# Optimization experiments

Measured on AMD Instinct MI355X. Metric: run time of the kernel, lower is better.

The kernel has to match this reference:

```python
import jax, jax.numpy as jnp
import numpy as np

NOISE_STD = 0.5
NOISE_VAR = NOISE_STD ** 2  # softmax temperature = 1 / noise_variance

N, C, H, W = 256, 3, 32, 32
M = 50000


def setup_inputs() -> dict:
    key = jax.random.key(0)
    k1, k2 = jax.random.split(key)
    x = jax.random.normal(k1, (N, C, H, W), dtype=jnp.float32)
    dataset = jax.random.normal(k2, (M, C, H, W), dtype=jnp.float32)
    return {"x": x, "dataset": dataset}


def reference(x, dataset):
    # Flatten: x -> [N, D], dataset -> [M, D]
    n = x.shape[0]
    input_shape = dataset.shape[1:]
    xf = x.reshape(n, -1)
    df = dataset.reshape(dataset.shape[0], -1)
    # scores = x . dataset^T / noise_variance, softmax over dataset axis
    scores = jnp.einsum("nd,md->nm", xf, df) / NOISE_VAR  # [N, M]
    w = jax.nn.softmax(scores, axis=-1)
    # Weighted average of dataset points: [N, D]
    out = jnp.einsum("nm,md->nd", w, df)
    return out.reshape((n,) + input_shape)
```

## Files before the change

### kernel.cpp

```cpp
#include <hip/hip_runtime.h>
#include <stdint.h>
#include <stddef.h>

#define N_Q 256
#define M_D 50000
#define K_D 3072
#define MTILE 64
#define BK 32
#define CAND_CAP 128
#define WINDOW 9.0f

typedef short bf16x8 __attribute__((ext_vector_type(8)));
typedef float f32x4 __attribute__((ext_vector_type(4)));

static __device__ inline unsigned short f2bf(float f) {
    unsigned int u = __float_as_uint(f);
    u += 0x7fffu + ((u >> 16) & 1u);
    return (unsigned short)(u >> 16);
}

__global__ __launch_bounds__(256) void cvt_x_kernel(const float* __restrict__ x,
                                                    short* __restrict__ xb) {
    int i = (blockIdx.x * 256 + threadIdx.x) * 4;
    float4 f = *(const float4*)(x + i);
    ushort4 o;
    o.x = f2bf(f.x); o.y = f2bf(f.y); o.z = f2bf(f.z); o.w = f2bf(f.w);
    *(ushort4*)(xb + i) = o;
}

__global__ __launch_bounds__(256) void gemm_scores(const short* __restrict__ xb,
                                                   const float* __restrict__ dset,
                                                   float* __restrict__ scores) {
    __shared__ __align__(16) short sA[N_Q * BK];
    __shared__ __align__(16) short sB[MTILE * BK];

    const int tid = threadIdx.x;
    const int w = tid >> 6;
    const int l = tid & 63;
    const int m0 = blockIdx.x * MTILE;

    f32x4 acc[4][4];
#pragma unroll
    for (int i = 0; i < 4; ++i)
#pragma unroll
        for (int j = 0; j < 4; ++j)
            acc[i][j] = (f32x4){0.f, 0.f, 0.f, 0.f};

    const int br = tid >> 2;
    const int bq = tid & 3;
    const bool bvalid = (m0 + br) < M_D;
    const float* bsrc = dset + (size_t)(m0 + br) * K_D + bq * 8;

    const int kk = (l >> 4) * 8;
    const int rA = l & 15;

    for (int kt = 0; kt < K_D / BK; ++kt) {
        __syncthreads();

#pragma unroll
        for (int j = 0; j < 4; ++j) {
            int c = j * 256 + tid;
            int row = c >> 2;
            int off = c & 3;
            bf16x8 v = *(const bf16x8*)(xb + (size_t)row * K_D + kt * BK + off * 8);
            *(bf16x8*)&sA[c * 8] = v;
        }
        {
            bf16x8 pk;
            if (bvalid) {
                const float* p = bsrc + kt * BK;
                float4 f0 = *(const float4*)p;
                float4 f1 = *(const float4*)(p + 4);
                pk[0] = (short)f2bf(f0.x); pk[1] = (short)f2bf(f0.y);
                pk[2] = (short)f2bf(f0.z); pk[3] = (short)f2bf(f0.w);
                pk[4] = (short)f2bf(f1.x); pk[5] = (short)f2bf(f1.y);
                pk[6] = (short)f2bf(f1.z); pk[7] = (short)f2bf(f1.w);
            } else {
                pk = (bf16x8){0, 0, 0, 0, 0, 0, 0, 0};
            }
            *(bf16x8*)&sB[br * BK + bq * 8] = pk;
        }
        __syncthreads();

        bf16x8 af[4], bfr[4];
#pragma unroll
        for (int ai = 0; ai < 4; ++ai)
            af[ai] = *(const bf16x8*)&sA[(w * 64 + ai * 16 + rA) * BK + kk];
#pragma unroll
        for (int bj = 0; bj < 4; ++bj)
            bfr[bj] = *(const bf16x8*)&sB[(bj * 16 + rA) * BK + kk];
#pragma unroll
        for (int ai = 0; ai < 4; ++ai)
#pragma unroll
            for (int bj = 0; bj < 4; ++bj)
                acc[ai][bj] = __builtin_amdgcn_mfma_f32_16x16x32_bf16(
                    af[ai], bfr[bj], acc[ai][bj], 0, 0, 0);
    }

    const int crow = (l >> 4) * 4;
    const int ccol = l & 15;
#pragma unroll
    for (int ai = 0; ai < 4; ++ai) {
#pragma unroll
        for (int bj = 0; bj < 4; ++bj) {
            int m = m0 + bj * 16 + ccol;
            if (m < M_D) {
#pragma unroll
                for (int r = 0; r < 4; ++r) {
                    int n = w * 64 + ai * 16 + crow + r;
                    scores[(size_t)n * M_D + m] = acc[ai][bj][r];
                }
            }
        }
    }
}

__global__ __launch_bounds__(256) void scan_rows(const float* __restrict__ scores,
                                                 int* __restrict__ cidx,
                                                 int* __restrict__ ccnt) {
    const int n = blockIdx.x;
    const int tid = threadIdx.x;
    const float4* row4 = (const float4*)(scores + (size_t)n * M_D);

    float mx = -3.0e38f;
    for (int m4 = tid; m4 < M_D / 4; m4 += 256) {
        float4 v = row4[m4];
        mx = fmaxf(mx, fmaxf(fmaxf(v.x, v.y), fmaxf(v.z, v.w)));
    }
#pragma unroll
    for (int off = 32; off > 0; off >>= 1) mx = fmaxf(mx, __shfl_down(mx, off));

    __shared__ float wred[4];
    __shared__ int cnt;
    if ((tid & 63) == 0) wred[tid >> 6] = mx;
    if (tid == 0) cnt = 0;
    __syncthreads();
    float rowmax = fmaxf(fmaxf(wred[0], wred[1]), fmaxf(wred[2], wred[3]));
    float thr = rowmax - WINDOW;

    for (int m4 = tid; m4 < M_D / 4; m4 += 256) {
        float4 v = row4[m4];
        if (v.x >= thr || v.y >= thr || v.z >= thr || v.w >= thr) {
            float e[4] = {v.x, v.y, v.z, v.w};
#pragma unroll
            for (int j = 0; j < 4; ++j) {
                if (e[j] >= thr) {
                    int p = atomicAdd(&cnt, 1);
                    if (p < CAND_CAP) cidx[n * CAND_CAP + p] = m4 * 4 + j;
                }
            }
        }
    }
    __syncthreads();
    if (tid == 0) ccnt[n] = cnt < CAND_CAP ? cnt : CAND_CAP;
}

__global__ __launch_bounds__(256) void finalize_rows(const float* __restrict__ x,
                                                     const float* __restrict__ dset,
                                                     const int* __restrict__ cidx,
                                                     const int* __restrict__ ccnt,
                                                     float* __restrict__ out) {
    const int n = blockIdx.x;
    const int tid = threadIdx.x;
    const int cnt = ccnt[n];

    __shared__ float L[CAND_CAP];
    __shared__ float wred[4];
    const float4* xr4 = (const float4*)(x + (size_t)n * K_D);

    for (int c = 0; c < cnt; ++c) {
        const float4* dr4 = (const float4*)(dset + (size_t)cidx[n * CAND_CAP + c] * K_D);
        float p = 0.f;
        for (int j = tid; j < K_D / 4; j += 256) {
            float4 a = xr4[j], b = dr4[j];
            p += a.x * b.x + a.y * b.y + a.z * b.z + a.w * b.w;
        }
#pragma unroll
        for (int off = 32; off > 0; off >>= 1) p += __shfl_down(p, off);
        if ((tid & 63) == 0) wred[tid >> 6] = p;
        __syncthreads();
        if (tid == 0) L[c] = 4.0f * (wred[0] + wred[1] + wred[2] + wred[3]);
        __syncthreads();
    }

    if (tid == 0) {
        float mx = -3.0e38f;
        for (int c = 0; c < cnt; ++c) mx = fmaxf(mx, L[c]);
        float s = 0.f;
        for (int c = 0; c < cnt; ++c) { float e = expf(L[c] - mx); L[c] = e; s += e; }
        float inv = 1.0f / s;
        for (int c = 0; c < cnt; ++c) L[c] *= inv;
    }
    __syncthreads();

    float4* out4 = (float4*)(out + (size_t)n * K_D);
    for (int j = tid; j < K_D / 4; j += 256) {
        float4 o = {0.f, 0.f, 0.f, 0.f};
        for (int c = 0; c < cnt; ++c) {
            float wc = L[c];
            float4 d = *(const float4*)(dset + (size_t)cidx[n * CAND_CAP + c] * K_D + j * 4);
            o.x += wc * d.x; o.y += wc * d.y; o.z += wc * d.z; o.w += wc * d.w;
        }
        out4[j] = o;
    }
}

extern "C" void kernel_launch(void* const* d_in, const int* in_sizes, int n_in,
                              void* d_out, int out_size, void* d_ws, size_t ws_size,
                              hipStream_t stream) {
    const float* x = (const float*)d_in[0];
    const float* dset = (const float*)d_in[1];
    float* out = (float*)d_out;

    char* ws = (char*)d_ws;
    short* xb = (short*)ws;
    float* scores = (float*)(ws + 1572864);
    int* cidx = (int*)(ws + 1572864 + 51200000);
    int* ccnt = (int*)(ws + 1572864 + 51200000 + 131072);

    cvt_x_kernel<<<768, 256, 0, stream>>>(x, xb);
    gemm_scores<<<(M_D + MTILE - 1) / MTILE, 256, 0, stream>>>(xb, dset, scores);
    scan_rows<<<N_Q, 256, 0, stream>>>(scores, cidx, ccnt);
    finalize_rows<<<N_Q, 256, 0, stream>>>(x, dset, cidx, ccnt, out);
}
```

Before: 961.5 us.

## Load A tile via global_load_lds, prefetch B before sync, fuse scan and finalize

The GEMM now loads the bf16 query tile straight from global memory into LDS with global_load_lds instead of staging it through registers. The dataset float loads are issued at the start of each k-iteration, and the barrier sits after the MFMAs so load latency overlaps the previous wait. The scan and finalize kernels are merged into one, with candidate indices kept in shared memory instead of a workspace buffer. This removes a kernel launch and the global round-trip for the candidate lists. The LDS layout for A has to match the lane-to-row mapping of global_load_lds, and correctness depends on it.

```diff
diff --git a/kernel.cpp b/kernel.cpp
--- a/kernel.cpp
+++ b/kernel.cpp
@@ -13,6 +13,9 @@
 typedef short bf16x8 __attribute__((ext_vector_type(8)));
 typedef float f32x4 __attribute__((ext_vector_type(4)));
 
+typedef const __attribute__((address_space(1))) void* gptr_as1;
+typedef __attribute__((address_space(3))) void* lptr_as3;
+
 static __device__ inline unsigned short f2bf(float f) {
     unsigned int u = __float_as_uint(f);
     u += 0x7fffu + ((u >> 16) & 1u);
@@ -51,26 +54,29 @@
     const bool bvalid = (m0 + br) < M_D;
     const float* bsrc = dset + (size_t)(m0 + br) * K_D + bq * 8;
 
+    const int arow_base = w * 16 + (l >> 2);
+    const int acol = (l & 3) * 8;
+
     const int kk = (l >> 4) * 8;
     const int rA = l & 15;
 
     for (int kt = 0; kt < K_D / BK; ++kt) {
-        __syncthreads();
-
+        float4 f0, f1;
+        if (bvalid) {
+            const float* p = bsrc + kt * BK;
+            f0 = *(const float4*)p;
+            f1 = *(const float4*)(p + 4);
+        }
 #pragma unroll
         for (int j = 0; j < 4; ++j) {
-            int c = j * 256 + tid;
-            int row = c >> 2;
-            int off = c & 3;
-            bf16x8 v = *(const bf16x8*)(xb + (size_t)row * K_D + kt * BK + off * 8);
-            *(bf16x8*)&sA[c * 8] = v;
+            const short* gp = xb + (size_t)(j * 64 + arow_base) * K_D + kt * BK + acol;
+            __builtin_amdgcn_global_load_lds((gptr_as1)gp,
+                                             (lptr_as3)(sA + j * 2048 + w * 512),
+                                             16, 0, 0);
         }
         {
             bf16x8 pk;
             if (bvalid) {
-                const float* p = bsrc + kt * BK;
-                float4 f0 = *(const float4*)p;
-                float4 f1 = *(const float4*)(p + 4);
                 pk[0] = (short)f2bf(f0.x); pk[1] = (short)f2bf(f0.y);
                 pk[2] = (short)f2bf(f0.z); pk[3] = (short)f2bf(f0.w);
                 pk[4] = (short)f2bf(f1.x); pk[5] = (short)f2bf(f1.y);
@@ -95,6 +101,7 @@
             for (int bj = 0; bj < 4; ++bj)
                 acc[ai][bj] = __builtin_amdgcn_mfma_f32_16x16x32_bf16(
                     af[ai], bfr[bj], acc[ai][bj], 0, 0, 0);
+        __syncthreads();
     }
 
     const int crow = (l >> 4) * 4;
@@ -115,12 +122,18 @@
     }
 }
 
-__global__ __launch_bounds__(256) void scan_rows(const float* __restrict__ scores,
-                                                 int* __restrict__ cidx,
-                                                 int* __restrict__ ccnt) {
+__global__ __launch_bounds__(256) void scan_finalize(const float* __restrict__ scores,
+                                                     const float* __restrict__ x,
+                                                     const float* __restrict__ dset,
+                                                     float* __restrict__ out) {
     const int n = blockIdx.x;
     const int tid = threadIdx.x;
     const float4* row4 = (const float4*)(scores + (size_t)n * M_D);
+
+    __shared__ float wred[4];
+    __shared__ int cnt;
+    __shared__ int cid[CAND_CAP];
+    __shared__ float L[CAND_CAP];
 
     float mx = -3.0e38f;
     for (int m4 = tid; m4 < M_D / 4; m4 += 256) {
@@ -129,9 +142,6 @@
     }
 #pragma unroll
     for (int off = 32; off > 0; off >>= 1) mx = fmaxf(mx, __shfl_down(mx, off));
-
-    __shared__ float wred[4];
-    __shared__ int cnt;
     if ((tid & 63) == 0) wred[tid >> 6] = mx;
     if (tid == 0) cnt = 0;
     __syncthreads();
@@ -146,30 +156,17 @@
             for (int j = 0; j < 4; ++j) {
                 if (e[j] >= thr) {
                     int p = atomicAdd(&cnt, 1);
-                    if (p < CAND_CAP) cidx[n * CAND_CAP + p] = m4 * 4 + j;
+                    if (p < CAND_CAP) cid[p] = m4 * 4 + j;
                 }
             }
         }
     }
     __syncthreads();
-    if (tid == 0) ccnt[n] = cnt < CAND_CAP ? cnt : CAND_CAP;
-}
-
-__global__ __launch_bounds__(256) void finalize_rows(const float* __restrict__ x,
-                                                     const float* __restrict__ dset,
-                                                     const int* __restrict__ cidx,
-                                                     const int* __restrict__ ccnt,
-                                                     float* __restrict__ out) {
-    const int n = blockIdx.x;
-    const int tid = threadIdx.x;
-    const int cnt = ccnt[n];
-
-    __shared__ float L[CAND_CAP];
-    __shared__ float wred[4];
+    const int c_n = cnt < CAND_CAP ? cnt : CAND_CAP;
+
     const float4* xr4 = (const float4*)(x + (size_t)n * K_D);
-
-    for (int c = 0; c < cnt; ++c) {
-        const float4* dr4 = (const float4*)(dset + (size_t)cidx[n * CAND_CAP + c] * K_D);
+    for (int c = 0; c < c_n; ++c) {
+        const float4* dr4 = (const float4*)(dset + (size_t)cid[c] * K_D);
         float p = 0.f;
         for (int j = tid; j < K_D / 4; j += 256) {
             float4 a = xr4[j], b = dr4[j];
@@ -184,21 +181,21 @@
     }
 
     if (tid == 0) {
-        float mx = -3.0e38f;
-        for (int c = 0; c < cnt; ++c) mx = fmaxf(mx, L[c]);
+        float m2 = -3.0e38f;
+        for (int c = 0; c < c_n; ++c) m2 = fmaxf(m2, L[c]);
         float s = 0.f;
-        for (int c = 0; c < cnt; ++c) { float e = expf(L[c] - mx); L[c] = e; s += e; }
+        for (int c = 0; c < c_n; ++c) { float e = expf(L[c] - m2); L[c] = e; s += e; }
         float inv = 1.0f / s;
-        for (int c = 0; c < cnt; ++c) L[c] *= inv;
+        for (int c = 0; c < c_n; ++c) L[c] *= inv;
     }
     __syncthreads();
 
     float4* out4 = (float4*)(out + (size_t)n * K_D);
     for (int j = tid; j < K_D / 4; j += 256) {
         float4 o = {0.f, 0.f, 0.f, 0.f};
-        for (int c = 0; c < cnt; ++c) {
+        for (int c = 0; c < c_n; ++c) {
             float wc = L[c];
-            float4 d = *(const float4*)(dset + (size_t)cidx[n * CAND_CAP + c] * K_D + j * 4);
+            float4 d = *(const float4*)(dset + (size_t)cid[c] * K_D + j * 4);
             o.x += wc * d.x; o.y += wc * d.y; o.z += wc * d.z; o.w += wc * d.w;
         }
         out4[j] = o;
@@ -215,11 +212,8 @@
     char* ws = (char*)d_ws;
     short* xb = (short*)ws;
     float* scores = (float*)(ws + 1572864);
-    int* cidx = (int*)(ws + 1572864 + 51200000);
-    int* ccnt = (int*)(ws + 1572864 + 51200000 + 131072);
 
     cvt_x_kernel<<<768, 256, 0, stream>>>(x, xb);
     gemm_scores<<<(M_D + MTILE - 1) / MTILE, 256, 0, stream>>>(xb, dset, scores);
-    scan_rows<<<N_Q, 256, 0, stream>>>(scores, cidx, ccnt);
-    finalize_rows<<<N_Q, 256, 0, stream>>>(x, dset, cidx, ccnt, out);
-}
+    scan_finalize<<<N_Q, 256, 0, stream>>>(scores, x, dset, out);
+}
```

Result: no change. 968.7 us (+0.7%).
